# Kernel optimization log

Hardware: AMD Instinct MI355X
Metric: run time of the kernel (lower is better)

Reference implementation:

```python
import jax, jax.numpy as jnp
import numpy as np

N_NODES = 50000
N_EDGES = 800000
D_IN = 256
D_HID = 256
D_OUT = 128


def setup_inputs() -> dict:
    key = jax.random.key(0)
    ks = jax.random.split(key, 6)
    z = jax.random.normal(ks[0], (N_NODES, D_IN), dtype=jnp.float32)
    edge_index = jax.random.randint(ks[1], (2, N_EDGES), 0, N_NODES, dtype=jnp.int32)
    W1 = jax.random.normal(ks[2], (D_IN, D_HID), dtype=jnp.float32) / np.sqrt(D_IN).astype(np.float32)
    b1 = jnp.zeros((D_HID,), dtype=jnp.float32)
    W2 = jax.random.normal(ks[3], (D_HID, D_OUT), dtype=jnp.float32) / np.sqrt(D_HID).astype(np.float32)
    b2 = jnp.zeros((D_OUT,), dtype=jnp.float32)
    return {"z": z, "edge_index": edge_index, "W1": W1, "b1": b1, "W2": W2, "b2": b2}


def _gcn_conv(x, W, b, src, dst, n_nodes):
    """GCNConv: x' = D^{-1/2} (A + I) D^{-1/2} (x W) + b (symmetric norm, self-loops)."""
    x = x @ W  # [n, d_out] dense transform first (as in PyG GCNConv)
    loop = jnp.arange(n_nodes, dtype=src.dtype)
    s = jnp.concatenate([src, loop])  # add self-loops
    d = jnp.concatenate([dst, loop])
    deg = jax.ops.segment_sum(jnp.ones(s.shape, dtype=x.dtype), d, num_segments=n_nodes)
    dinv = jnp.where(deg > 0, jax.lax.rsqrt(deg), 0.0)
    norm = dinv[s] * dinv[d]  # per-edge symmetric normalization
    msgs = x[s] * norm[:, None]  # gather + scale
    out = jax.ops.segment_sum(msgs, d, num_segments=n_nodes)  # scatter-add
    return out + b


def reference(z, edge_index, W1, b1, W2, b2):
    src, dst = edge_index[0], edge_index[1]
    n = z.shape[0]
    h = jax.nn.relu(_gcn_conv(z, W1, b1, src, dst, n))
    return _gcn_conv(h, W2, b2, src, dst, n)
```

## Files before the change

### kernel.cpp

```cpp
#include <hip/hip_runtime.h>


#define N_NODES 50000
#define N_EDGES 800000
#define D_IN    256
#define D_HID   256
#define D_OUT   128

typedef unsigned int uint32;
typedef unsigned short u16;

typedef __attribute__((ext_vector_type(8))) short bf16x8;
typedef __attribute__((ext_vector_type(4))) float f32x4;

__device__ __forceinline__ u16 f2bf_rne(float f) {
    union { float f; uint32 u; } c; c.f = f;
    uint32 u = c.u;
    u += 0x7FFFu + ((u >> 16) & 1u);
    return (u16)(u >> 16);
}
__device__ __forceinline__ float bf_lo(uint32 p) {
    union { uint32 u; float f; } c; c.u = p << 16; return c.f;
}
__device__ __forceinline__ float bf_hi(uint32 p) {
    union { uint32 u; float f; } c; c.u = p & 0xFFFF0000u; return c.f;
}


__global__ __launch_bounds__(256) void cvt_bf16_kernel(const float* __restrict__ in,
                                                       u16* __restrict__ out, int n) {
    int i = (blockIdx.x * blockDim.x + threadIdx.x) * 8;
    if (i < n) {
        float4 a = *(const float4*)(in + i);
        float4 b = *(const float4*)(in + i + 4);
        uint4 pk;
        pk.x = (uint32)f2bf_rne(a.x) | ((uint32)f2bf_rne(a.y) << 16);
        pk.y = (uint32)f2bf_rne(a.z) | ((uint32)f2bf_rne(a.w) << 16);
        pk.z = (uint32)f2bf_rne(b.x) | ((uint32)f2bf_rne(b.y) << 16);
        pk.w = (uint32)f2bf_rne(b.z) | ((uint32)f2bf_rne(b.w) << 16);
        *(uint4*)(out + i) = pk;
    }
}

__global__ __launch_bounds__(256) void wt_kernel(const float* __restrict__ W,
                                                 u16* __restrict__ WT, int K, int N) {
    int idx = blockIdx.x * 256 + threadIdx.x;
    if (idx < K * N) {
        int nrow = idx / K;
        int kcol = idx - nrow * K;
        WT[idx] = f2bf_rne(W[(size_t)kcol * N + nrow]);
    }
}


__global__ void degree_kernel(const int* __restrict__ dst, int* __restrict__ cnt, int n_edges) {
    int i = blockIdx.x * blockDim.x + threadIdx.x;
    if (i < n_edges) atomicAdd(&cnt[dst[i]], 1);
}

__global__ void dinv_kernel(const int* __restrict__ cnt, float* __restrict__ dinv, int n) {
    int i = blockIdx.x * blockDim.x + threadIdx.x;
    if (i < n) dinv[i] = rsqrtf((float)(cnt[i] + 1));
}

__global__ __launch_bounds__(256) void block_sum_kernel(const int* __restrict__ cnt,
                                                        int* __restrict__ bsum, int n) {
    int b = blockIdx.x, t = threadIdx.x;
    int i = b * 256 + t;
    int v = (i < n) ? cnt[i] : 0;
    #pragma unroll
    for (int off = 32; off >= 1; off >>= 1) v += __shfl_down(v, off, 64);
    __shared__ int ws[4];
    if ((t & 63) == 0) ws[t >> 6] = v;
    __syncthreads();
    if (t == 0) bsum[b] = ws[0] + ws[1] + ws[2] + ws[3];
}

__global__ __launch_bounds__(256) void scan_partials_kernel(const int* __restrict__ bsum,
                                                            int* __restrict__ boff,
                                                            int* __restrict__ row_ptr,
                                                            int nb, int n) {
    int t = threadIdx.x;
    int v = (t < nb) ? bsum[t] : 0;
    int lane = t & 63, w = t >> 6;
    int x = v;
    #pragma unroll
    for (int off = 1; off < 64; off <<= 1) {
        int u = __shfl_up(x, off, 64);
        if (lane >= off) x += u;
    }
    __shared__ int ws[4];
    if (lane == 63) ws[w] = x;
    __syncthreads();
    int base = 0;
    for (int i = 0; i < w; ++i) base += ws[i];
    int incl = base + x;
    if (t < nb) boff[t] = incl - v;
    if (t == 255) row_ptr[n] = incl;
}

__global__ __launch_bounds__(256) void scan_write_kernel(const int* __restrict__ cnt,
                                                         const int* __restrict__ boff,
                                                         int* __restrict__ row_ptr,
                                                         int* __restrict__ cursor, int n) {
    int b = blockIdx.x, t = threadIdx.x;
    int i = b * 256 + t;
    int v = (i < n) ? cnt[i] : 0;
    int lane = t & 63, w = t >> 6;
    int x = v;
    #pragma unroll
    for (int off = 1; off < 64; off <<= 1) {
        int u = __shfl_up(x, off, 64);
        if (lane >= off) x += u;
    }
    __shared__ int ws[4];
    if (lane == 63) ws[w] = x;
    __syncthreads();
    int base = boff[b];
    for (int i2 = 0; i2 < w; ++i2) base += ws[i2];
    int excl = base + (x - v);
    if (i < n) { row_ptr[i] = excl; cursor[i] = excl; }
}

__global__ void fill_kernel(const int* __restrict__ src, const int* __restrict__ dst,
                            int* __restrict__ cursor, int* __restrict__ col, int n_edges) {
    int i = blockIdx.x * blockDim.x + threadIdx.x;
    if (i < n_edges) {
        int d = dst[i];
        int s = src[i];
        int pos = atomicAdd(&cursor[d], 1);
        col[pos] = s;
    }
}


template <int NT>
__global__ __launch_bounds__(256, 4) void gemm_bf16_kernel(const u16* __restrict__ A,
                                                           const u16* __restrict__ BT,
                                                           u16* __restrict__ C, int M) {
    const int K = 256;
    __shared__ short As[128 * 32];
    __shared__ short Bs[128 * 32];

    const int m0 = blockIdx.x * 128;
    const int n0 = blockIdx.y * 128;
    const int t  = threadIdx.x;
    const int w  = t >> 6;
    const int lane = t & 63;
    const int lm = lane & 15;
    const int lq = lane >> 4;
    const int wm = w & 1;
    const int wn = w >> 1;

    f32x4 acc[4][4] = {};

    for (int k0 = 0; k0 < K; k0 += 32) {
        #pragma unroll
        for (int j = 0; j < 2; ++j) {
            int c = w * 128 + j * 64 + lane;
            int row = c >> 2;
            int kc = k0 + (c & 3) * 8;
            int gm = m0 + row; if (gm >= M) gm = M - 1;
            const u16* gpa = A  + (size_t)gm * K + kc;
            const u16* gpb = BT + (size_t)(n0 + row) * K + kc;
            __builtin_amdgcn_global_load_lds(
                (const __attribute__((address_space(1))) void*)gpa,
                (__attribute__((address_space(3))) void*)(As + (w * 128 + j * 64) * 8),
                16, 0, 0);
            __builtin_amdgcn_global_load_lds(
                (const __attribute__((address_space(1))) void*)gpb,
                (__attribute__((address_space(3))) void*)(Bs + (w * 128 + j * 64) * 8),
                16, 0, 0);
        }
        __syncthreads();

        bf16x8 af[4], bf[4];
        #pragma unroll
        for (int mt = 0; mt < 4; ++mt)
            af[mt] = *(const bf16x8*)&As[(wm * 64 + mt * 16 + lm) * 32 + lq * 8];
        #pragma unroll
        for (int nt = 0; nt < 4; ++nt)
            bf[nt] = *(const bf16x8*)&Bs[(wn * 64 + nt * 16 + lm) * 32 + lq * 8];

        #pragma unroll
        for (int mt = 0; mt < 4; ++mt)
            #pragma unroll
            for (int nt = 0; nt < 4; ++nt)
                acc[mt][nt] = __builtin_amdgcn_mfma_f32_16x16x32_bf16(
                    af[mt], bf[nt], acc[mt][nt], 0, 0, 0);

        __syncthreads();
    }

    #pragma unroll
    for (int mt = 0; mt < 4; ++mt) {
        #pragma unroll
        for (int r = 0; r < 4; ++r) {
            int gm = m0 + wm * 64 + mt * 16 + lq * 4 + r;
            if (gm < M) {
                #pragma unroll
                for (int nt = 0; nt < 4; ++nt) {
                    int gn = n0 + wn * 64 + nt * 16 + lm;
                    C[(size_t)gm * NT + gn] = f2bf_rne(acc[mt][nt][r]);
                }
            }
        }
    }
}


template <int D, bool RELU, bool OUTBF>
__global__ __launch_bounds__(256) void aggregate_kernel(const u16* __restrict__ x,
                                                        const int* __restrict__ row_ptr,
                                                        const int* __restrict__ col,
                                                        const float* __restrict__ dinv,
                                                        const float* __restrict__ bias,
                                                        void* __restrict__ outp, int n_nodes) {
    constexpr int VPL = D / 64;
    int wave = (blockIdx.x * blockDim.x + threadIdx.x) >> 6;
    int lane = threadIdx.x & 63;
    if (wave >= n_nodes) return;
    const int node = wave;
    const int c0 = lane * VPL;

    float di = dinv[node];
    float acc[4][VPL] = {};

    {
        float w = di * di;
        const u16* xs = x + (size_t)node * D + c0;
        if constexpr (VPL == 4) {
            uint2 p = *(const uint2*)xs;
            acc[0][0] = bf_lo(p.x) * w;
            acc[0][1] = bf_hi(p.x) * w;
            acc[0][2] = bf_lo(p.y) * w;
            acc[0][3] = bf_hi(p.y) * w;
        } else {
            uint32 p = *(const uint32*)xs;
            acc[0][0] = bf_lo(p) * w;
            acc[0][1] = bf_hi(p) * w;
        }
    }

    int e0 = row_ptr[node], e1 = row_ptr[node + 1];
    int e = e0;
    for (; e + 4 <= e1; e += 4) {
        #pragma unroll
        for (int u = 0; u < 4; ++u) {
            int s  = col[e + u];
            float w = dinv[s] * di;
            const u16* xs = x + (size_t)s * D + c0;
            if constexpr (VPL == 4) {
                uint2 p = *(const uint2*)xs;
                acc[u][0] = fmaf(bf_lo(p.x), w, acc[u][0]);
                acc[u][1] = fmaf(bf_hi(p.x), w, acc[u][1]);
                acc[u][2] = fmaf(bf_lo(p.y), w, acc[u][2]);
                acc[u][3] = fmaf(bf_hi(p.y), w, acc[u][3]);
            } else {
                uint32 p = *(const uint32*)xs;
                acc[u][0] = fmaf(bf_lo(p), w, acc[u][0]);
                acc[u][1] = fmaf(bf_hi(p), w, acc[u][1]);
            }
        }
    }
    for (; e < e1; ++e) {
        int s  = col[e];
        float w = dinv[s] * di;
        const u16* xs = x + (size_t)s * D + c0;
        if constexpr (VPL == 4) {
            uint2 p = *(const uint2*)xs;
            acc[0][0] = fmaf(bf_lo(p.x), w, acc[0][0]);
            acc[0][1] = fmaf(bf_hi(p.x), w, acc[0][1]);
            acc[0][2] = fmaf(bf_lo(p.y), w, acc[0][2]);
            acc[0][3] = fmaf(bf_hi(p.y), w, acc[0][3]);
        } else {
            uint32 p = *(const uint32*)xs;
            acc[0][0] = fmaf(bf_lo(p), w, acc[0][0]);
            acc[0][1] = fmaf(bf_hi(p), w, acc[0][1]);
        }
    }

    float v[VPL];
    #pragma unroll
    for (int j = 0; j < VPL; ++j) {
        float s = acc[0][j] + acc[1][j] + acc[2][j] + acc[3][j] + bias[c0 + j];
        v[j] = RELU ? fmaxf(s, 0.0f) : s;
    }

    if constexpr (OUTBF) {
        u16* op = (u16*)outp + (size_t)node * D + c0;
        if constexpr (VPL == 4) {
            uint2 pk;
            pk.x = (uint32)f2bf_rne(v[0]) | ((uint32)f2bf_rne(v[1]) << 16);
            pk.y = (uint32)f2bf_rne(v[2]) | ((uint32)f2bf_rne(v[3]) << 16);
            *(uint2*)op = pk;
        } else {
            *(uint32*)op = (uint32)f2bf_rne(v[0]) | ((uint32)f2bf_rne(v[1]) << 16);
        }
    } else {
        float* op = (float*)outp + (size_t)node * D + c0;
        #pragma unroll
        for (int j = 0; j < VPL; ++j) op[j] = v[j];
    }
}


extern "C" void kernel_launch(void* const* d_in, const int* in_sizes, int n_in,
                              void* d_out, int out_size, void* d_ws, size_t ws_size,
                              hipStream_t stream) {
    const float* z  = (const float*)d_in[0];
    const int*   ei = (const int*)d_in[1];
    const float* W1 = (const float*)d_in[2];
    const float* b1 = (const float*)d_in[3];
    const float* W2 = (const float*)d_in[4];
    const float* b2 = (const float*)d_in[5];
    float* out = (float*)d_out;

    const int Nn = N_NODES, E = N_EDGES;
    const int* srcp = ei;
    const int* dstp = ei + E;

    char* ws = (char*)d_ws;
    size_t off = 0;
    auto alloc = [&](size_t bytes) -> char* {
        char* p = ws + off;
        off += (bytes + 511) & ~(size_t)511;
        return p;
    };
    u16*   zb     = (u16*)  alloc((size_t)Nn * D_IN * 2);
    u16*   w1t    = (u16*)  alloc((size_t)D_IN * D_HID * 2);
    u16*   w2t    = (u16*)  alloc((size_t)D_HID * D_OUT * 2);
    u16*   x1b    = (u16*)  alloc((size_t)Nn * D_HID * 2);
    u16*   hb     = (u16*)  alloc((size_t)Nn * D_HID * 2);
    u16*   h2b    = (u16*)  alloc((size_t)Nn * D_OUT * 2);
    int*   cnt    = (int*)  alloc((size_t)Nn * 4);
    float* dinv   = (float*)alloc((size_t)Nn * 4);
    int*   row_ptr= (int*)  alloc((size_t)(Nn + 1) * 4);
    int*   cursor = (int*)  alloc((size_t)Nn * 4);
    int*   col    = (int*)  alloc((size_t)E * 4);
    int*   bsum   = (int*)  alloc(256 * 4);
    int*   boff   = (int*)  alloc(256 * 4);

    const int nb = (Nn + 255) / 256;

    cvt_bf16_kernel<<<(Nn * D_IN / 8 + 255) / 256, 256, 0, stream>>>(z, zb, Nn * D_IN);
    wt_kernel<<<(D_IN * D_HID + 255) / 256, 256, 0, stream>>>(W1, w1t, D_IN, D_HID);
    wt_kernel<<<(D_HID * D_OUT + 255) / 256, 256, 0, stream>>>(W2, w2t, D_HID, D_OUT);

    hipMemsetAsync(cnt, 0, (size_t)Nn * 4, stream);
    degree_kernel<<<(E + 255) / 256, 256, 0, stream>>>(dstp, cnt, E);
    dinv_kernel<<<(Nn + 255) / 256, 256, 0, stream>>>(cnt, dinv, Nn);
    block_sum_kernel<<<nb, 256, 0, stream>>>(cnt, bsum, Nn);
    scan_partials_kernel<<<1, 256, 0, stream>>>(bsum, boff, row_ptr, nb, Nn);
    scan_write_kernel<<<nb, 256, 0, stream>>>(cnt, boff, row_ptr, cursor, Nn);
    fill_kernel<<<(E + 255) / 256, 256, 0, stream>>>(srcp, dstp, cursor, col, E);

    {
        dim3 grid((Nn + 127) / 128, D_HID / 128);
        gemm_bf16_kernel<D_HID><<<grid, 256, 0, stream>>>(zb, w1t, x1b, Nn);
    }
    {
        int blocks = (Nn * 64 + 255) / 256;
        aggregate_kernel<D_HID, true, true><<<blocks, 256, 0, stream>>>(x1b, row_ptr, col, dinv, b1, hb, Nn);
    }

    {
        dim3 grid((Nn + 127) / 128, D_OUT / 128);
        gemm_bf16_kernel<D_OUT><<<grid, 256, 0, stream>>>(hb, w2t, h2b, Nn);
    }
    {
        int blocks = (Nn * 64 + 255) / 256;
        aggregate_kernel<D_OUT, false, false><<<blocks, 256, 0, stream>>>(h2b, row_ptr, col, dinv, b2, out, Nn);
    }
}
```

Before: 330.1 us.

## Fuse preprocessing and CSR build into one persistent kernel with grid barriers

Replaces nine small launches (bf16 conversion, weight transposes, degree count, dinv, three-stage scan, fill) with one 512-block persistent kernel. Phases are separated by atomic-counter grid barriers, and the scan uses 98-node chunks per block so 512 partials fit one block scan. This removes launch overhead and inter-kernel gaps. It relies on all 512 blocks being co-resident, otherwise the barriers deadlock. Fewer threads also do the large conversion and atomic work in grid-stride loops.

Measured after the change: 721.4 us. 119% more time.

```diff
diff --git a/kernel.cpp b/kernel.cpp
--- a/kernel.cpp
+++ b/kernel.cpp
@@ -7,6 +7,9 @@
 #define D_HID   256
 #define D_OUT   128
 
+#define NBLK  512
+#define CHUNK 98
+
 typedef unsigned int uint32;
 typedef unsigned short u16;
 
@@ -26,106 +29,125 @@
     union { uint32 u; float f; } c; c.u = p & 0xFFFF0000u; return c.f;
 }
 
-
-__global__ __launch_bounds__(256) void cvt_bf16_kernel(const float* __restrict__ in,
-                                                       u16* __restrict__ out, int n) {
-    int i = (blockIdx.x * blockDim.x + threadIdx.x) * 8;
-    if (i < n) {
-        float4 a = *(const float4*)(in + i);
-        float4 b = *(const float4*)(in + i + 4);
-        uint4 pk;
-        pk.x = (uint32)f2bf_rne(a.x) | ((uint32)f2bf_rne(a.y) << 16);
-        pk.y = (uint32)f2bf_rne(a.z) | ((uint32)f2bf_rne(a.w) << 16);
-        pk.z = (uint32)f2bf_rne(b.x) | ((uint32)f2bf_rne(b.y) << 16);
-        pk.w = (uint32)f2bf_rne(b.z) | ((uint32)f2bf_rne(b.w) << 16);
-        *(uint4*)(out + i) = pk;
-    }
-}
-
-__global__ __launch_bounds__(256) void wt_kernel(const float* __restrict__ W,
-                                                 u16* __restrict__ WT, int K, int N) {
-    int idx = blockIdx.x * 256 + threadIdx.x;
-    if (idx < K * N) {
-        int nrow = idx / K;
-        int kcol = idx - nrow * K;
-        WT[idx] = f2bf_rne(W[(size_t)kcol * N + nrow]);
-    }
-}
-
-
-__global__ void degree_kernel(const int* __restrict__ dst, int* __restrict__ cnt, int n_edges) {
-    int i = blockIdx.x * blockDim.x + threadIdx.x;
-    if (i < n_edges) atomicAdd(&cnt[dst[i]], 1);
-}
-
-__global__ void dinv_kernel(const int* __restrict__ cnt, float* __restrict__ dinv, int n) {
-    int i = blockIdx.x * blockDim.x + threadIdx.x;
-    if (i < n) dinv[i] = rsqrtf((float)(cnt[i] + 1));
-}
-
-__global__ __launch_bounds__(256) void block_sum_kernel(const int* __restrict__ cnt,
-                                                        int* __restrict__ bsum, int n) {
-    int b = blockIdx.x, t = threadIdx.x;
-    int i = b * 256 + t;
-    int v = (i < n) ? cnt[i] : 0;
-    #pragma unroll
-    for (int off = 32; off >= 1; off >>= 1) v += __shfl_down(v, off, 64);
-    __shared__ int ws[4];
-    if ((t & 63) == 0) ws[t >> 6] = v;
+__device__ __forceinline__ int aload(const int* p) {
+    return __hip_atomic_load(p, __ATOMIC_ACQUIRE, __HIP_MEMORY_SCOPE_AGENT);
+}
+__device__ __forceinline__ void astore(int* p, int v) {
+    __hip_atomic_store(p, v, __ATOMIC_RELEASE, __HIP_MEMORY_SCOPE_AGENT);
+}
+
+__device__ __forceinline__ void grid_bar(int* bar, int idx) {
     __syncthreads();
-    if (t == 0) bsum[b] = ws[0] + ws[1] + ws[2] + ws[3];
-}
-
-__global__ __launch_bounds__(256) void scan_partials_kernel(const int* __restrict__ bsum,
-                                                            int* __restrict__ boff,
-                                                            int* __restrict__ row_ptr,
-                                                            int nb, int n) {
-    int t = threadIdx.x;
-    int v = (t < nb) ? bsum[t] : 0;
-    int lane = t & 63, w = t >> 6;
+    __threadfence();
+    if (threadIdx.x == 0) {
+        __hip_atomic_fetch_add(&bar[idx], 1, __ATOMIC_ACQ_REL, __HIP_MEMORY_SCOPE_AGENT);
+        while (__hip_atomic_load(&bar[idx], __ATOMIC_ACQUIRE, __HIP_MEMORY_SCOPE_AGENT) < NBLK)
+            __builtin_amdgcn_s_sleep(8);
+    }
+    __syncthreads();
+    __threadfence();
+}
+
+__device__ __forceinline__ int block_incl_scan(int v, int* wsum) {
+    int t = threadIdx.x, lane = t & 63, w = t >> 6;
     int x = v;
     #pragma unroll
     for (int off = 1; off < 64; off <<= 1) {
         int u = __shfl_up(x, off, 64);
         if (lane >= off) x += u;
     }
-    __shared__ int ws[4];
-    if (lane == 63) ws[w] = x;
+    if (lane == 63) wsum[w] = x;
     __syncthreads();
     int base = 0;
-    for (int i = 0; i < w; ++i) base += ws[i];
-    int incl = base + x;
-    if (t < nb) boff[t] = incl - v;
-    if (t == 255) row_ptr[n] = incl;
-}
-
-__global__ __launch_bounds__(256) void scan_write_kernel(const int* __restrict__ cnt,
-                                                         const int* __restrict__ boff,
-                                                         int* __restrict__ row_ptr,
-                                                         int* __restrict__ cursor, int n) {
-    int b = blockIdx.x, t = threadIdx.x;
-    int i = b * 256 + t;
-    int v = (i < n) ? cnt[i] : 0;
-    int lane = t & 63, w = t >> 6;
-    int x = v;
-    #pragma unroll
-    for (int off = 1; off < 64; off <<= 1) {
-        int u = __shfl_up(x, off, 64);
-        if (lane >= off) x += u;
-    }
-    __shared__ int ws[4];
-    if (lane == 63) ws[w] = x;
+    for (int i = 0; i < w; ++i) base += wsum[i];
     __syncthreads();
-    int base = boff[b];
-    for (int i2 = 0; i2 < w; ++i2) base += ws[i2];
-    int excl = base + (x - v);
-    if (i < n) { row_ptr[i] = excl; cursor[i] = excl; }
-}
-
-__global__ void fill_kernel(const int* __restrict__ src, const int* __restrict__ dst,
-                            int* __restrict__ cursor, int* __restrict__ col, int n_edges) {
-    int i = blockIdx.x * blockDim.x + threadIdx.x;
-    if (i < n_edges) {
+    return base + x;
+}
+
+
+__global__ __launch_bounds__(256) void csr_build_kernel(
+        const float* __restrict__ z, const int* __restrict__ src,
+        const int* __restrict__ dst,
+        const float* __restrict__ W1, const float* __restrict__ W2,
+        u16* __restrict__ zb, u16* __restrict__ w1t, u16* __restrict__ w2t,
+        int* __restrict__ cnt, float* __restrict__ dinv,
+        int* __restrict__ row_ptr, int* __restrict__ cursor,
+        int* __restrict__ col, int* __restrict__ bsum, int* __restrict__ boff,
+        int* __restrict__ bar) {
+    const int t = threadIdx.x;
+    const int b = blockIdx.x;
+    const int g = b * 256 + t;
+    const int GT = NBLK * 256;
+    __shared__ int wsum[4];
+
+    for (int idx = g; idx < D_IN * D_HID + D_HID * D_OUT; idx += GT) {
+        if (idx < D_IN * D_HID) {
+            int nrow = idx >> 8, kcol = idx & 255;
+            w1t[idx] = f2bf_rne(W1[kcol * D_HID + nrow]);
+        } else {
+            int j = idx - D_IN * D_HID;
+            int nrow = j >> 8, kcol = j & 255;
+            w2t[j] = f2bf_rne(W2[kcol * D_OUT + nrow]);
+        }
+    }
+    for (int c = g; c < N_NODES * D_IN / 8; c += GT) {
+        int i = c * 8;
+        float4 a = *(const float4*)(z + i);
+        float4 d = *(const float4*)(z + i + 4);
+        uint4 pk;
+        pk.x = (uint32)f2bf_rne(a.x) | ((uint32)f2bf_rne(a.y) << 16);
+        pk.y = (uint32)f2bf_rne(a.z) | ((uint32)f2bf_rne(a.w) << 16);
+        pk.z = (uint32)f2bf_rne(d.x) | ((uint32)f2bf_rne(d.y) << 16);
+        pk.w = (uint32)f2bf_rne(d.z) | ((uint32)f2bf_rne(d.w) << 16);
+        *(uint4*)(zb + i) = pk;
+    }
+    for (int i = g; i < N_EDGES; i += GT) atomicAdd(&cnt[dst[i]], 1);
+    grid_bar(bar, 0);
+
+    {
+        int node = b * CHUNK + t;
+        int v = 0;
+        if (t < CHUNK && node < N_NODES) {
+            v = aload(&cnt[node]);
+            dinv[node] = rsqrtf((float)(v + 1));
+        }
+        int lane = t & 63, w = t >> 6;
+        int r = v;
+        #pragma unroll
+        for (int off = 32; off >= 1; off >>= 1) r += __shfl_down(r, off, 64);
+        if (lane == 0) wsum[w] = r;
+        __syncthreads();
+        if (t == 0) astore(&bsum[b], wsum[0] + wsum[1] + wsum[2] + wsum[3]);
+        __syncthreads();
+    }
+    grid_bar(bar, 1);
+
+    if (b == 0) {
+        int v0 = aload(&bsum[2 * t]);
+        int v1 = aload(&bsum[2 * t + 1]);
+        int s = v0 + v1;
+        int incl = block_incl_scan(s, wsum);
+        int excl = incl - s;
+        astore(&boff[2 * t], excl);
+        astore(&boff[2 * t + 1], excl + v0);
+        if (t == 255) row_ptr[N_NODES] = incl;
+    }
+    grid_bar(bar, 2);
+
+    {
+        int node = b * CHUNK + t;
+        int v = (t < CHUNK && node < N_NODES) ? aload(&cnt[node]) : 0;
+        int incl = block_incl_scan(v, wsum);
+        int excl = incl - v;
+        int base = aload(&boff[b]);
+        if (t < CHUNK && node < N_NODES) {
+            row_ptr[node] = base + excl;
+            astore(&cursor[node], base + excl);
+        }
+    }
+    grid_bar(bar, 3);
+
+    for (int i = g; i < N_EDGES; i += GT) {
         int d = dst[i];
         int s = src[i];
         int pos = atomicAdd(&cursor[d], 1);
@@ -334,26 +356,20 @@
     u16*   hb     = (u16*)  alloc((size_t)Nn * D_HID * 2);
     u16*   h2b    = (u16*)  alloc((size_t)Nn * D_OUT * 2);
     int*   cnt    = (int*)  alloc((size_t)Nn * 4);
+    int*   bar    = (int*)  alloc(64);
     float* dinv   = (float*)alloc((size_t)Nn * 4);
     int*   row_ptr= (int*)  alloc((size_t)(Nn + 1) * 4);
     int*   cursor = (int*)  alloc((size_t)Nn * 4);
     int*   col    = (int*)  alloc((size_t)E * 4);
-    int*   bsum   = (int*)  alloc(256 * 4);
-    int*   boff   = (int*)  alloc(256 * 4);
-
-    const int nb = (Nn + 255) / 256;
-
-    cvt_bf16_kernel<<<(Nn * D_IN / 8 + 255) / 256, 256, 0, stream>>>(z, zb, Nn * D_IN);
-    wt_kernel<<<(D_IN * D_HID + 255) / 256, 256, 0, stream>>>(W1, w1t, D_IN, D_HID);
-    wt_kernel<<<(D_HID * D_OUT + 255) / 256, 256, 0, stream>>>(W2, w2t, D_HID, D_OUT);
-
-    hipMemsetAsync(cnt, 0, (size_t)Nn * 4, stream);
-    degree_kernel<<<(E + 255) / 256, 256, 0, stream>>>(dstp, cnt, E);
-    dinv_kernel<<<(Nn + 255) / 256, 256, 0, stream>>>(cnt, dinv, Nn);
-    block_sum_kernel<<<nb, 256, 0, stream>>>(cnt, bsum, Nn);
-    scan_partials_kernel<<<1, 256, 0, stream>>>(bsum, boff, row_ptr, nb, Nn);
-    scan_write_kernel<<<nb, 256, 0, stream>>>(cnt, boff, row_ptr, cursor, Nn);
-    fill_kernel<<<(E + 255) / 256, 256, 0, stream>>>(srcp, dstp, cursor, col, E);
+    int*   bsum   = (int*)  alloc(NBLK * 4);
+    int*   boff   = (int*)  alloc(NBLK * 4);
+
+    size_t zspan = (size_t)((char*)bar - (char*)cnt) + 512;
+    hipMemsetAsync(cnt, 0, zspan, stream);
+
+    csr_build_kernel<<<NBLK, 256, 0, stream>>>(z, srcp, dstp, W1, W2,
+                                               zb, w1t, w2t, cnt, dinv,
+                                               row_ptr, cursor, col, bsum, boff, bar);
 
     {
         dim3 grid((Nn + 127) / 128, D_HID / 128);
@@ -363,7 +379,6 @@
         int blocks = (Nn * 64 + 255) / 256;
         aggregate_kernel<D_HID, true, true><<<blocks, 256, 0, stream>>>(x1b, row_ptr, col, dinv, b1, hb, Nn);
     }
-
     {
         dim3 grid((Nn + 127) / 128, D_OUT / 128);
         gemm_bf16_kernel<D_OUT><<<grid, 256, 0, stream>>>(hb, w2t, h2b, Nn);
```

## Fuse preprocessing kernels and split hidden-layer aggregation across feature halves

Applied to the files above, without the earlier changes.

Merges the z bf16 conversion, both weight transposes and the degree atomic count into one grid-stride prep kernel, and folds the dinv computation into the block-sum kernel. This removes several kernel launches. The first-layer aggregation now splits the 256-wide feature dimension across two blocks per group of four nodes, so each lane handles 2 values instead of 4. That gives more parallelism and smaller per-lane loads, but each edge's col index and dinv are read twice. A fixed 1024-block prep grid may leave the large conversion with fewer in-flight threads than before.

After: 334.5 us. About the same (+1.3%).

```diff
diff --git a/kernel.cpp b/kernel.cpp
--- a/kernel.cpp
+++ b/kernel.cpp
@@ -27,51 +27,57 @@
 }
 
 
-__global__ __launch_bounds__(256) void cvt_bf16_kernel(const float* __restrict__ in,
-                                                       u16* __restrict__ out, int n) {
-    int i = (blockIdx.x * blockDim.x + threadIdx.x) * 8;
-    if (i < n) {
-        float4 a = *(const float4*)(in + i);
-        float4 b = *(const float4*)(in + i + 4);
+__global__ __launch_bounds__(256) void prep_kernel(const float* __restrict__ z,
+                                                   const int* __restrict__ dst,
+                                                   const float* __restrict__ W1,
+                                                   const float* __restrict__ W2,
+                                                   u16* __restrict__ zb,
+                                                   u16* __restrict__ w1t,
+                                                   u16* __restrict__ w2t,
+                                                   int* __restrict__ cnt) {
+    const int g = blockIdx.x * 256 + threadIdx.x;
+    const int GT = gridDim.x * 256;
+
+    for (int c = g; c < N_NODES * D_IN / 8; c += GT) {
+        int i = c * 8;
+        float4 a = *(const float4*)(z + i);
+        float4 d = *(const float4*)(z + i + 4);
         uint4 pk;
         pk.x = (uint32)f2bf_rne(a.x) | ((uint32)f2bf_rne(a.y) << 16);
         pk.y = (uint32)f2bf_rne(a.z) | ((uint32)f2bf_rne(a.w) << 16);
-        pk.z = (uint32)f2bf_rne(b.x) | ((uint32)f2bf_rne(b.y) << 16);
-        pk.w = (uint32)f2bf_rne(b.z) | ((uint32)f2bf_rne(b.w) << 16);
-        *(uint4*)(out + i) = pk;
-    }
-}
-
-__global__ __launch_bounds__(256) void wt_kernel(const float* __restrict__ W,
-                                                 u16* __restrict__ WT, int K, int N) {
-    int idx = blockIdx.x * 256 + threadIdx.x;
-    if (idx < K * N) {
-        int nrow = idx / K;
-        int kcol = idx - nrow * K;
-        WT[idx] = f2bf_rne(W[(size_t)kcol * N + nrow]);
-    }
-}
-
-
-__global__ void degree_kernel(const int* __restrict__ dst, int* __restrict__ cnt, int n_edges) {
-    int i = blockIdx.x * blockDim.x + threadIdx.x;
-    if (i < n_edges) atomicAdd(&cnt[dst[i]], 1);
-}
-
-__global__ void dinv_kernel(const int* __restrict__ cnt, float* __restrict__ dinv, int n) {
-    int i = blockIdx.x * blockDim.x + threadIdx.x;
-    if (i < n) dinv[i] = rsqrtf((float)(cnt[i] + 1));
-}
+        pk.z = (uint32)f2bf_rne(d.x) | ((uint32)f2bf_rne(d.y) << 16);
+        pk.w = (uint32)f2bf_rne(d.z) | ((uint32)f2bf_rne(d.w) << 16);
+        *(uint4*)(zb + i) = pk;
+    }
+    for (int idx = g; idx < D_IN * D_HID + D_HID * D_OUT; idx += GT) {
+        if (idx < D_IN * D_HID) {
+            int nrow = idx >> 8, kcol = idx & 255;
+            w1t[idx] = f2bf_rne(W1[kcol * D_HID + nrow]);
+        } else {
+            int j = idx - D_IN * D_HID;
+            int nrow = j >> 8, kcol = j & 255;
+            w2t[j] = f2bf_rne(W2[kcol * D_OUT + nrow]);
+        }
+    }
+    for (int i = g; i < N_EDGES; i += GT) atomicAdd(&cnt[dst[i]], 1);
+}
+
 
 __global__ __launch_bounds__(256) void block_sum_kernel(const int* __restrict__ cnt,
+                                                        float* __restrict__ dinv,
                                                         int* __restrict__ bsum, int n) {
     int b = blockIdx.x, t = threadIdx.x;
     int i = b * 256 + t;
-    int v = (i < n) ? cnt[i] : 0;
-    #pragma unroll
-    for (int off = 32; off >= 1; off >>= 1) v += __shfl_down(v, off, 64);
+    int v = 0;
+    if (i < n) {
+        v = cnt[i];
+        dinv[i] = rsqrtf((float)(v + 1));
+    }
+    int r = v;
+    #pragma unroll
+    for (int off = 32; off >= 1; off >>= 1) r += __shfl_down(r, off, 64);
     __shared__ int ws[4];
-    if ((t & 63) == 0) ws[t >> 6] = v;
+    if ((t & 63) == 0) ws[t >> 6] = r;
     __syncthreads();
     if (t == 0) bsum[b] = ws[0] + ws[1] + ws[2] + ws[3];
 }
@@ -209,19 +215,21 @@
 }
 
 
-template <int D, bool RELU, bool OUTBF>
+template <int D, int NSPLIT, bool RELU, bool OUTBF>
 __global__ __launch_bounds__(256) void aggregate_kernel(const u16* __restrict__ x,
                                                         const int* __restrict__ row_ptr,
                                                         const int* __restrict__ col,
                                                         const float* __restrict__ dinv,
                                                         const float* __restrict__ bias,
                                                         void* __restrict__ outp, int n_nodes) {
-    constexpr int VPL = D / 64;
-    int wave = (blockIdx.x * blockDim.x + threadIdx.x) >> 6;
-    int lane = threadIdx.x & 63;
-    if (wave >= n_nodes) return;
-    const int node = wave;
-    const int c0 = lane * VPL;
+    constexpr int DP  = D / NSPLIT;
+    constexpr int VPL = DP / 64;
+    const int b = blockIdx.x;
+    const int part = b % NSPLIT;
+    const int node = (b / NSPLIT) * 4 + (threadIdx.x >> 6);
+    const int lane = threadIdx.x & 63;
+    if (node >= n_nodes) return;
+    const int c0 = part * DP + lane * VPL;
 
     float di = dinv[node];
     float acc[4][VPL] = {};
@@ -343,14 +351,9 @@
 
     const int nb = (Nn + 255) / 256;
 
-    cvt_bf16_kernel<<<(Nn * D_IN / 8 + 255) / 256, 256, 0, stream>>>(z, zb, Nn * D_IN);
-    wt_kernel<<<(D_IN * D_HID + 255) / 256, 256, 0, stream>>>(W1, w1t, D_IN, D_HID);
-    wt_kernel<<<(D_HID * D_OUT + 255) / 256, 256, 0, stream>>>(W2, w2t, D_HID, D_OUT);
-
     hipMemsetAsync(cnt, 0, (size_t)Nn * 4, stream);
-    degree_kernel<<<(E + 255) / 256, 256, 0, stream>>>(dstp, cnt, E);
-    dinv_kernel<<<(Nn + 255) / 256, 256, 0, stream>>>(cnt, dinv, Nn);
-    block_sum_kernel<<<nb, 256, 0, stream>>>(cnt, bsum, Nn);
+    prep_kernel<<<1024, 256, 0, stream>>>(z, dstp, W1, W2, zb, w1t, w2t, cnt);
+    block_sum_kernel<<<nb, 256, 0, stream>>>(cnt, dinv, bsum, Nn);
     scan_partials_kernel<<<1, 256, 0, stream>>>(bsum, boff, row_ptr, nb, Nn);
     scan_write_kernel<<<nb, 256, 0, stream>>>(cnt, boff, row_ptr, cursor, Nn);
     fill_kernel<<<(E + 255) / 256, 256, 0, stream>>>(srcp, dstp, cursor, col, E);
@@ -360,8 +363,8 @@
         gemm_bf16_kernel<D_HID><<<grid, 256, 0, stream>>>(zb, w1t, x1b, Nn);
     }
     {
-        int blocks = (Nn * 64 + 255) / 256;
-        aggregate_kernel<D_HID, true, true><<<blocks, 256, 0, stream>>>(x1b, row_ptr, col, dinv, b1, hb, Nn);
+        int blocks = 2 * ((Nn + 3) / 4);
+        aggregate_kernel<D_HID, 2, true, true><<<blocks, 256, 0, stream>>>(x1b, row_ptr, col, dinv, b1, hb, Nn);
     }
 
     {
@@ -369,7 +372,7 @@
         gemm_bf16_kernel<D_OUT><<<grid, 256, 0, stream>>>(hb, w2t, h2b, Nn);
     }
     {
-        int blocks = (Nn * 64 + 255) / 256;
-        aggregate_kernel<D_OUT, false, false><<<blocks, 256, 0, stream>>>(h2b, row_ptr, col, dinv, b2, out, Nn);
-    }
-}
+        int blocks = (Nn + 3) / 4;
+        aggregate_kernel<D_OUT, 1, false, false><<<blocks, 256, 0, stream>>>(h2b, row_ptr, col, dinv, b2, out, Nn);
+    }
+}
```
